# Kernel tuning notes

Measured on AMD Instinct MI355X. Metric: run time of the kernel, lower is better.

The kernel has to match this reference:

```python
import jax, jax.numpy as jnp
import numpy as np

N = 100000
E = 600000
D = 128
D_OUT = 128
NUM_CONV = 3


def setup_inputs() -> dict:
    key = jax.random.key(0)
    k0, k1, k2, k3, k4, k5 = jax.random.split(key, 6)
    x = jax.random.normal(k0, (N, D), dtype=jnp.float32)
    edge_index = jax.random.randint(k1, (2, E), 0, N, dtype=jnp.int64)
    s = 1.0 / np.sqrt(D)
    W = jax.random.uniform(k2, (D, D), minval=-s, maxval=s, dtype=jnp.float32)
    b = jax.random.uniform(k3, (D,), minval=-s, maxval=s, dtype=jnp.float32)
    W_out = jax.random.uniform(k4, (D, D_OUT), minval=-s, maxval=s, dtype=jnp.float32)
    b_out = jax.random.uniform(k5, (D_OUT,), minval=-s, maxval=s, dtype=jnp.float32)
    return {"x": x, "edge_index": edge_index, "W": W, "b": b,
            "W_out": W_out, "b_out": b_out}


def reference(x, edge_index, W, b, W_out, b_out):
    src, dst = edge_index[0], edge_index[1]
    for _ in range(NUM_CONV):
        # gather messages from src nodes, scatter-sum into dst nodes
        agg = jax.ops.segment_sum(x[src], dst, num_segments=N)  # [N, D]
        x = jax.nn.relu(agg @ W + b)  # shared GCNLayer weights + ReLU
    return x @ W_out + b_out  # [N, D_OUT]
```

## Files before the change

### kernel.cpp

```cpp
#include <hip/hip_runtime.h>

#define NN 100000
#define NE 600000
#define DD 128

typedef __attribute__((ext_vector_type(8))) short bf16x8;
typedef __attribute__((ext_vector_type(4))) float f32x4;

__device__ __forceinline__ ushort f2bf(float f) {
  uint u = __float_as_uint(f);
  return (ushort)((u + 0x7FFF + ((u >> 16) & 1)) >> 16);
}
__device__ __forceinline__ float bf2f(ushort h) { return __uint_as_float(((uint)h) << 16); }


__global__ __launch_bounds__(256) void zero_kernel(int* __restrict__ p, int n) {
  int i = blockIdx.x * 256 + threadIdx.x;
  if (i < n) p[i] = 0;
}

__global__ __launch_bounds__(256) void count_deg(const int* __restrict__ dst, int* __restrict__ cnt) {
  int e = blockIdx.x * 256 + threadIdx.x;
  if (e < NE) atomicAdd(&cnt[dst[e]], 1);
}

__global__ __launch_bounds__(1024) void scan_partial(const int* __restrict__ cnt,
                                                     int* __restrict__ rowptr,
                                                     int* __restrict__ bsum) {
  __shared__ int tmp[2][1024];
  int t = threadIdx.x;
  int g = blockIdx.x * 1024 + t;
  int v = (g < NN) ? cnt[g] : 0;
  tmp[0][t] = v;
  __syncthreads();
  int pb = 0;
  for (int off = 1; off < 1024; off <<= 1) {
    int nv = tmp[pb][t] + ((t >= off) ? tmp[pb][t - off] : 0);
    tmp[1 - pb][t] = nv;
    pb ^= 1;
    __syncthreads();
  }
  int incl = tmp[pb][t];
  if (g < NN) rowptr[g] = incl - v;
  if (t == 1023) bsum[blockIdx.x] = incl;
}

__global__ __launch_bounds__(128) void scan_sums(int* __restrict__ bsum, int nb) {
  __shared__ int s[128];
  int t = threadIdx.x;
  s[t] = (t < nb) ? bsum[t] : 0;
  __syncthreads();
  if (t == 0) {
    int run = 0;
    for (int j = 0; j < nb; ++j) { int v = s[j]; s[j] = run; run += v; }
  }
  __syncthreads();
  if (t < nb) bsum[t] = s[t];
}

__global__ __launch_bounds__(256) void scan_add(int* __restrict__ rowptr, const int* __restrict__ bsum) {
  int g = blockIdx.x * 256 + threadIdx.x;
  if (g < NN) rowptr[g] += bsum[g >> 10];
  if (g == 0) rowptr[NN] = NE;
}

__global__ __launch_bounds__(256) void fill_csr(const int* __restrict__ src, const int* __restrict__ dst,
                                                const int* __restrict__ rowptr, int* __restrict__ cur,
                                                int* __restrict__ srcidx) {
  int e = blockIdx.x * 256 + threadIdx.x;
  if (e < NE) {
    int d = dst[e];
    int pos = atomicAdd(&cur[d], 1);
    srcidx[rowptr[d] + pos] = src[e];
  }
}


__global__ __launch_bounds__(256) void wprep(const float* __restrict__ W, const float* __restrict__ Wo,
                                             ushort* __restrict__ WTh, ushort* __restrict__ WTl,
                                             ushort* __restrict__ WToh, ushort* __restrict__ WTol) {
  int i = blockIdx.x * 256 + threadIdx.x;
  int j = i & 16383;
  int k = j >> 7, n = j & 127;
  float w = (i < 16384) ? W[j] : Wo[j];
  ushort h = f2bf(w);
  ushort lo = f2bf(w - bf2f(h));
  int o = n * 128 + k;
  if (i < 16384) { WTh[o] = h; WTl[o] = lo; }
  else           { WToh[o] = h; WTol[o] = lo; }
}


__global__ __launch_bounds__(256) void aggregate(const float* __restrict__ y,
                                                 const int* __restrict__ rowptr,
                                                 const int* __restrict__ srcidx,
                                                 ushort* __restrict__ Ah, ushort* __restrict__ Al) {
  int grp  = (int)((blockIdx.x * 256 + threadIdx.x) >> 5);
  int lane = threadIdx.x & 31;
  if (grp >= NN) return;
  int beg = rowptr[grp], end = rowptr[grp + 1];
  float4 a0 = make_float4(0.f, 0.f, 0.f, 0.f);
  float4 a1 = make_float4(0.f, 0.f, 0.f, 0.f);
  int j = beg;
  for (; j + 2 <= end; j += 2) {
    int s0 = srcidx[j], s1 = srcidx[j + 1];
    float4 v0 = *(const float4*)(y + (size_t)s0 * DD + lane * 4);
    float4 v1 = *(const float4*)(y + (size_t)s1 * DD + lane * 4);
    a0.x += v0.x; a0.y += v0.y; a0.z += v0.z; a0.w += v0.w;
    a1.x += v1.x; a1.y += v1.y; a1.z += v1.z; a1.w += v1.w;
  }
  if (j < end) {
    int s0 = srcidx[j];
    float4 v0 = *(const float4*)(y + (size_t)s0 * DD + lane * 4);
    a0.x += v0.x; a0.y += v0.y; a0.z += v0.z; a0.w += v0.w;
  }
  float v[4] = {a0.x + a1.x, a0.y + a1.y, a0.z + a1.z, a0.w + a1.w};
  ushort h[4], l[4];
  #pragma unroll
  for (int r = 0; r < 4; ++r) { h[r] = f2bf(v[r]); l[r] = f2bf(v[r] - bf2f(h[r])); }
  uint2 hh, ll;
  hh.x = (uint)h[0] | ((uint)h[1] << 16); hh.y = (uint)h[2] | ((uint)h[3] << 16);
  ll.x = (uint)l[0] | ((uint)l[1] << 16); ll.y = (uint)l[2] | ((uint)l[3] << 16);
  *(uint2*)(Ah + (size_t)grp * DD + lane * 4) = hh;
  *(uint2*)(Al + (size_t)grp * DD + lane * 4) = ll;
}


template <int MODE>
__global__ __launch_bounds__(256, 3) void gemm_mfma(const ushort* Ah, const ushort* Al,
                                                    const ushort* __restrict__ Bh, const ushort* __restrict__ Bl,
                                                    const float* __restrict__ bias,
                                                    float* Cf, ushort* Ch, ushort* Cl, int nrows) {
  __shared__ ushort BHs[128 * 64];
  __shared__ ushort BLs[128 * 64];
  int t = threadIdx.x;
  int w = t >> 6, l = t & 63;
  int lrow = l & 15, g = l >> 4;
  int m0 = blockIdx.x * 128 + w * 32;

  f32x4 acc[2][8];
  #pragma unroll
  for (int rt = 0; rt < 2; ++rt)
    #pragma unroll
    for (int ct = 0; ct < 8; ++ct) acc[rt][ct] = (f32x4){0.f, 0.f, 0.f, 0.f};

  #pragma unroll
  for (int p = 0; p < 2; ++p) {
    #pragma unroll
    for (int i = 0; i < 4; ++i) {
      int c = t + i * 256;
      int n = c >> 3, k8 = c & 7;
      int gsrc = n * 128 + p * 64 + k8 * 8;
      int dsw  = n * 64 + (((k8 * 16) ^ ((n & 7) << 4)) >> 1);
      *(uint4*)(&BHs[dsw]) = *(const uint4*)(Bh + gsrc);
      *(uint4*)(&BLs[dsw]) = *(const uint4*)(Bl + gsrc);
    }
    __syncthreads();

    #pragma unroll
    for (int kb = 0; kb < 2; ++kb) {
      int kgl = (p * 2 + kb) * 32 + g * 8;
      bf16x8 ah[2], al[2];
      #pragma unroll
      for (int rt = 0; rt < 2; ++rt) {
        int row = m0 + rt * 16 + lrow; if (row >= nrows) row = nrows - 1;
        ah[rt] = *(const bf16x8*)(Ah + (size_t)row * DD + kgl);
        al[rt] = *(const bf16x8*)(Al + (size_t)row * DD + kgl);
      }
      int kloc = kb * 64 + g * 16;
      int swz = (lrow & 7) << 4;
      #pragma unroll
      for (int ct = 0; ct < 8; ++ct) {
        int off = (ct * 16 + lrow) * 64 + ((kloc ^ swz) >> 1);
        bf16x8 bh = *(const bf16x8*)(&BHs[off]);
        bf16x8 bl = *(const bf16x8*)(&BLs[off]);
        #pragma unroll
        for (int rt = 0; rt < 2; ++rt) {
          acc[rt][ct] = __builtin_amdgcn_mfma_f32_16x16x32_bf16(ah[rt], bh, acc[rt][ct], 0, 0, 0);
          acc[rt][ct] = __builtin_amdgcn_mfma_f32_16x16x32_bf16(ah[rt], bl, acc[rt][ct], 0, 0, 0);
          acc[rt][ct] = __builtin_amdgcn_mfma_f32_16x16x32_bf16(al[rt], bh, acc[rt][ct], 0, 0, 0);
        }
      }
    }
    __syncthreads();
  }

  float bb[8];
  #pragma unroll
  for (int ct = 0; ct < 8; ++ct) bb[ct] = bias[ct * 16 + lrow];
  #pragma unroll
  for (int rt = 0; rt < 2; ++rt) {
    #pragma unroll
    for (int r = 0; r < 4; ++r) {
      int row = m0 + rt * 16 + g * 4 + r;
      if (row < nrows) {
        #pragma unroll
        for (int ct = 0; ct < 8; ++ct) {
          float v = acc[rt][ct][r] + bb[ct];
          if (MODE != 2) v = fmaxf(v, 0.f);
          int col = ct * 16 + lrow;
          if (MODE == 1) {
            ushort h = f2bf(v);
            Ch[(size_t)row * DD + col] = h;
            Cl[(size_t)row * DD + col] = f2bf(v - bf2f(h));
          } else {
            Cf[(size_t)row * DD + col] = v;
          }
        }
      }
    }
  }
}


extern "C" void kernel_launch(void* const* d_in, const int* in_sizes, int n_in,
                              void* d_out, int out_size, void* d_ws, size_t ws_size,
                              hipStream_t stream) {
  const float* x     = (const float*)d_in[0];
  const int*   ei    = (const int*)d_in[1];
  const float* W     = (const float*)d_in[2];
  const float* b     = (const float*)d_in[3];
  const float* W_out = (const float*)d_in[4];
  const float* b_out = (const float*)d_in[5];
  float*       out   = (float*)d_out;

  const int* src = ei;
  const int* dst = ei + NE;

  char* ws = (char*)d_ws;
  int*    rowptr = (int*)(ws + 0);
  int*    cnt    = (int*)(ws + 400128);
  int*    bsum   = (int*)(ws + 800256);
  int*    srcidx = (int*)(ws + 802304);
  ushort* WTh    = (ushort*)(ws + 3202304);
  ushort* WTl    = (ushort*)(ws + 3235072);
  ushort* WToh   = (ushort*)(ws + 3267840);
  ushort* WTol   = (ushort*)(ws + 3300608);
  ushort* Ahb    = (ushort*)(ws + 3333376);
  ushort* Alb    = (ushort*)(ws + 28933376);
  float*  yf     = (float*)(ws + 54533376);

  const int nb_scan = (NN + 1023) / 1024;

  zero_kernel<<<(NN + 255) / 256, 256, 0, stream>>>(cnt, NN);
  count_deg<<<(NE + 255) / 256, 256, 0, stream>>>(dst, cnt);
  scan_partial<<<nb_scan, 1024, 0, stream>>>(cnt, rowptr, bsum);
  scan_sums<<<1, 128, 0, stream>>>(bsum, nb_scan);
  scan_add<<<(NN + 255) / 256, 256, 0, stream>>>(rowptr, bsum);
  zero_kernel<<<(NN + 255) / 256, 256, 0, stream>>>(cnt, NN);
  fill_csr<<<(NE + 255) / 256, 256, 0, stream>>>(src, dst, rowptr, cnt, srcidx);
  wprep<<<128, 256, 0, stream>>>(W, W_out, WTh, WTl, WToh, WTol);

  const int aggBlocks  = (NN * 32 + 255) / 256;
  const int gemmBlocks = (NN + 127) / 128;

  aggregate<<<aggBlocks, 256, 0, stream>>>(x, rowptr, srcidx, Ahb, Alb);
  gemm_mfma<0><<<gemmBlocks, 256, 0, stream>>>(Ahb, Alb, WTh, WTl, b, yf, nullptr, nullptr, NN);
  aggregate<<<aggBlocks, 256, 0, stream>>>(yf, rowptr, srcidx, Ahb, Alb);
  gemm_mfma<0><<<gemmBlocks, 256, 0, stream>>>(Ahb, Alb, WTh, WTl, b, yf, nullptr, nullptr, NN);
  aggregate<<<aggBlocks, 256, 0, stream>>>(yf, rowptr, srcidx, Ahb, Alb);
  gemm_mfma<1><<<gemmBlocks, 256, 0, stream>>>(Ahb, Alb, WTh, WTl, b, nullptr, Ahb, Alb, NN);
  gemm_mfma<2><<<gemmBlocks, 256, 0, stream>>>(Ahb, Alb, WToh, WTol, b_out, out, nullptr, nullptr, NN);
}
```

Measured before the change: 413.6 us.

## Fuse aggregation with GEMM per layer and merge setup kernels

Each GCN layer now runs as one kernel: a 512-thread block gathers and sums neighbour rows for 128 nodes, splits them into bf16 hi/lo parts and stores them in swizzled LDS, then runs the MFMA GEMM straight from LDS with bias and ReLU. The last layer also chains the output projection inside the same kernel. This removes the round-trip of the bf16 hi/lo intermediates through global memory and cuts several launches. Setup is trimmed too: the weight prep is merged into the counter-zeroing kernel, and the CSR fill counts down with atomicSub so the second zeroing pass can go. In exchange, B fragments now come from global/L2 instead of LDS, each block holds 64KB of LDS, which limits occupancy, and the gather phase gives each warp more rows to process serially.

```diff
diff --git a/kernel.cpp b/kernel.cpp
--- a/kernel.cpp
+++ b/kernel.cpp
@@ -14,9 +14,23 @@
 __device__ __forceinline__ float bf2f(ushort h) { return __uint_as_float(((uint)h) << 16); }
 
 
-__global__ __launch_bounds__(256) void zero_kernel(int* __restrict__ p, int n) {
+__global__ __launch_bounds__(256) void zero_wprep(int* __restrict__ cnt,
+                                                  const float* __restrict__ W, const float* __restrict__ Wo,
+                                                  ushort* __restrict__ WTh, ushort* __restrict__ WTl,
+                                                  ushort* __restrict__ WToh, ushort* __restrict__ WTol) {
   int i = blockIdx.x * 256 + threadIdx.x;
-  if (i < n) p[i] = 0;
+  if (i < NN) cnt[i] = 0;
+  int j = i - NN;
+  if (j >= 0 && j < 32768) {
+    int q = j & 16383;
+    int k = q >> 7, n = q & 127;
+    float w = (j < 16384) ? W[q] : Wo[q];
+    ushort h = f2bf(w);
+    ushort lo = f2bf(w - bf2f(h));
+    int o = n * 128 + k;
+    if (j < 16384) { WTh[o] = h; WTl[o] = lo; }
+    else           { WToh[o] = h; WTol[o] = lo; }
+  }
 }
 
 __global__ __launch_bounds__(256) void count_deg(const int* __restrict__ dst, int* __restrict__ cnt) {
@@ -70,143 +84,149 @@
   int e = blockIdx.x * 256 + threadIdx.x;
   if (e < NE) {
     int d = dst[e];
-    int pos = atomicAdd(&cur[d], 1);
+    int pos = atomicSub(&cur[d], 1) - 1;
     srcidx[rowptr[d] + pos] = src[e];
   }
 }
 
 
-__global__ __launch_bounds__(256) void wprep(const float* __restrict__ W, const float* __restrict__ Wo,
-                                             ushort* __restrict__ WTh, ushort* __restrict__ WTl,
-                                             ushort* __restrict__ WToh, ushort* __restrict__ WTol) {
-  int i = blockIdx.x * 256 + threadIdx.x;
-  int j = i & 16383;
-  int k = j >> 7, n = j & 127;
-  float w = (i < 16384) ? W[j] : Wo[j];
-  ushort h = f2bf(w);
-  ushort lo = f2bf(w - bf2f(h));
-  int o = n * 128 + k;
-  if (i < 16384) { WTh[o] = h; WTl[o] = lo; }
-  else           { WToh[o] = h; WTol[o] = lo; }
-}
-
-
-__global__ __launch_bounds__(256) void aggregate(const float* __restrict__ y,
-                                                 const int* __restrict__ rowptr,
-                                                 const int* __restrict__ srcidx,
-                                                 ushort* __restrict__ Ah, ushort* __restrict__ Al) {
-  int grp  = (int)((blockIdx.x * 256 + threadIdx.x) >> 5);
-  int lane = threadIdx.x & 31;
-  if (grp >= NN) return;
-  int beg = rowptr[grp], end = rowptr[grp + 1];
-  float4 a0 = make_float4(0.f, 0.f, 0.f, 0.f);
-  float4 a1 = make_float4(0.f, 0.f, 0.f, 0.f);
-  int j = beg;
-  for (; j + 2 <= end; j += 2) {
-    int s0 = srcidx[j], s1 = srcidx[j + 1];
-    float4 v0 = *(const float4*)(y + (size_t)s0 * DD + lane * 4);
-    float4 v1 = *(const float4*)(y + (size_t)s1 * DD + lane * 4);
-    a0.x += v0.x; a0.y += v0.y; a0.z += v0.z; a0.w += v0.w;
-    a1.x += v1.x; a1.y += v1.y; a1.z += v1.z; a1.w += v1.w;
-  }
-  if (j < end) {
-    int s0 = srcidx[j];
-    float4 v0 = *(const float4*)(y + (size_t)s0 * DD + lane * 4);
-    a0.x += v0.x; a0.y += v0.y; a0.z += v0.z; a0.w += v0.w;
-  }
-  float v[4] = {a0.x + a1.x, a0.y + a1.y, a0.z + a1.z, a0.w + a1.w};
-  ushort h[4], l[4];
-  #pragma unroll
-  for (int r = 0; r < 4; ++r) { h[r] = f2bf(v[r]); l[r] = f2bf(v[r] - bf2f(h[r])); }
-  uint2 hh, ll;
-  hh.x = (uint)h[0] | ((uint)h[1] << 16); hh.y = (uint)h[2] | ((uint)h[3] << 16);
-  ll.x = (uint)l[0] | ((uint)l[1] << 16); ll.y = (uint)l[2] | ((uint)l[3] << 16);
-  *(uint2*)(Ah + (size_t)grp * DD + lane * 4) = hh;
-  *(uint2*)(Al + (size_t)grp * DD + lane * 4) = ll;
-}
-
-
-template <int MODE>
-__global__ __launch_bounds__(256, 3) void gemm_mfma(const ushort* Ah, const ushort* Al,
-                                                    const ushort* __restrict__ Bh, const ushort* __restrict__ Bl,
-                                                    const float* __restrict__ bias,
-                                                    float* Cf, ushort* Ch, ushort* Cl, int nrows) {
-  __shared__ ushort BHs[128 * 64];
-  __shared__ ushort BLs[128 * 64];
-  int t = threadIdx.x;
+template <bool LAST>
+__global__ __launch_bounds__(512, 4) void layer_fused(
+    const float* __restrict__ yin,
+    const int* __restrict__ rowptr, const int* __restrict__ srcidx,
+    const ushort* __restrict__ Bh, const ushort* __restrict__ Bl,
+    const float* __restrict__ bias,
+    const ushort* __restrict__ B2h, const ushort* __restrict__ B2l,
+    const float* __restrict__ bias2,
+    float* __restrict__ yout) {
+  __shared__ ushort AH[128 * 128];
+  __shared__ ushort AL[128 * 128];
+  int t  = threadIdx.x;
+  int m0 = blockIdx.x * 128;
+
+  {
+    int gp = t >> 5, lane = t & 31;
+    for (int rr = 0; rr < 8; ++rr) {
+      int row  = gp * 8 + rr;
+      int node = m0 + row;
+      float4 a0 = make_float4(0.f, 0.f, 0.f, 0.f);
+      float4 a1 = make_float4(0.f, 0.f, 0.f, 0.f);
+      if (node < NN) {
+        int beg = rowptr[node], end = rowptr[node + 1];
+        int j = beg;
+        for (; j + 2 <= end; j += 2) {
+          int s0 = srcidx[j], s1 = srcidx[j + 1];
+          float4 v0 = *(const float4*)(yin + (size_t)s0 * DD + lane * 4);
+          float4 v1 = *(const float4*)(yin + (size_t)s1 * DD + lane * 4);
+          a0.x += v0.x; a0.y += v0.y; a0.z += v0.z; a0.w += v0.w;
+          a1.x += v1.x; a1.y += v1.y; a1.z += v1.z; a1.w += v1.w;
+        }
+        if (j < end) {
+          int s0 = srcidx[j];
+          float4 v0 = *(const float4*)(yin + (size_t)s0 * DD + lane * 4);
+          a0.x += v0.x; a0.y += v0.y; a0.z += v0.z; a0.w += v0.w;
+        }
+      }
+      float v[4] = {a0.x + a1.x, a0.y + a1.y, a0.z + a1.z, a0.w + a1.w};
+      ushort h[4], l[4];
+      #pragma unroll
+      for (int r = 0; r < 4; ++r) { h[r] = f2bf(v[r]); l[r] = f2bf(v[r] - bf2f(h[r])); }
+      uint2 hh, ll;
+      hh.x = (uint)h[0] | ((uint)h[1] << 16); hh.y = (uint)h[2] | ((uint)h[3] << 16);
+      ll.x = (uint)l[0] | ((uint)l[1] << 16); ll.y = (uint)l[2] | ((uint)l[3] << 16);
+      int boff = row * 256 + ((lane * 8) ^ ((row & 7) << 4));
+      *(uint2*)((char*)AH + boff) = hh;
+      *(uint2*)((char*)AL + boff) = ll;
+    }
+  }
+  __syncthreads();
+
   int w = t >> 6, l = t & 63;
   int lrow = l & 15, g = l >> 4;
-  int m0 = blockIdx.x * 128 + w * 32;
-
-  f32x4 acc[2][8];
+  int rbase = w * 16;
+
+  bf16x8 ah[4], al[4];
   #pragma unroll
-  for (int rt = 0; rt < 2; ++rt)
-    #pragma unroll
-    for (int ct = 0; ct < 8; ++ct) acc[rt][ct] = (f32x4){0.f, 0.f, 0.f, 0.f};
-
+  for (int kb = 0; kb < 4; ++kb) {
+    int row  = rbase + lrow;
+    int boff = row * 256 + ((kb * 64 + g * 16) ^ ((row & 7) << 4));
+    ah[kb] = *(const bf16x8*)((char*)AH + boff);
+    al[kb] = *(const bf16x8*)((char*)AL + boff);
+  }
+  f32x4 acc[8];
   #pragma unroll
-  for (int p = 0; p < 2; ++p) {
-    #pragma unroll
-    for (int i = 0; i < 4; ++i) {
-      int c = t + i * 256;
-      int n = c >> 3, k8 = c & 7;
-      int gsrc = n * 128 + p * 64 + k8 * 8;
-      int dsw  = n * 64 + (((k8 * 16) ^ ((n & 7) << 4)) >> 1);
-      *(uint4*)(&BHs[dsw]) = *(const uint4*)(Bh + gsrc);
-      *(uint4*)(&BLs[dsw]) = *(const uint4*)(Bl + gsrc);
-    }
+  for (int ct = 0; ct < 8; ++ct) acc[ct] = (f32x4){0.f, 0.f, 0.f, 0.f};
+
+  #pragma unroll
+  for (int ct = 0; ct < 8; ++ct) {
+    int nrow = ct * 16 + lrow;
+    #pragma unroll
+    for (int kb = 0; kb < 4; ++kb) {
+      bf16x8 bh = *(const bf16x8*)(Bh + (size_t)nrow * 128 + kb * 32 + g * 8);
+      bf16x8 bl = *(const bf16x8*)(Bl + (size_t)nrow * 128 + kb * 32 + g * 8);
+      acc[ct] = __builtin_amdgcn_mfma_f32_16x16x32_bf16(ah[kb], bh, acc[ct], 0, 0, 0);
+      acc[ct] = __builtin_amdgcn_mfma_f32_16x16x32_bf16(ah[kb], bl, acc[ct], 0, 0, 0);
+      acc[ct] = __builtin_amdgcn_mfma_f32_16x16x32_bf16(al[kb], bh, acc[ct], 0, 0, 0);
+    }
+  }
+
+  if (!LAST) {
+    #pragma unroll
+    for (int ct = 0; ct < 8; ++ct) {
+      float bb = bias[ct * 16 + lrow];
+      #pragma unroll
+      for (int r = 0; r < 4; ++r) {
+        int row = m0 + rbase + g * 4 + r;
+        if (row < NN) {
+          float v = fmaxf(acc[ct][r] + bb, 0.f);
+          yout[(size_t)row * DD + ct * 16 + lrow] = v;
+        }
+      }
+    }
+  } else {
     __syncthreads();
-
-    #pragma unroll
-    for (int kb = 0; kb < 2; ++kb) {
-      int kgl = (p * 2 + kb) * 32 + g * 8;
-      bf16x8 ah[2], al[2];
-      #pragma unroll
-      for (int rt = 0; rt < 2; ++rt) {
-        int row = m0 + rt * 16 + lrow; if (row >= nrows) row = nrows - 1;
-        ah[rt] = *(const bf16x8*)(Ah + (size_t)row * DD + kgl);
-        al[rt] = *(const bf16x8*)(Al + (size_t)row * DD + kgl);
-      }
-      int kloc = kb * 64 + g * 16;
-      int swz = (lrow & 7) << 4;
-      #pragma unroll
-      for (int ct = 0; ct < 8; ++ct) {
-        int off = (ct * 16 + lrow) * 64 + ((kloc ^ swz) >> 1);
-        bf16x8 bh = *(const bf16x8*)(&BHs[off]);
-        bf16x8 bl = *(const bf16x8*)(&BLs[off]);
-        #pragma unroll
-        for (int rt = 0; rt < 2; ++rt) {
-          acc[rt][ct] = __builtin_amdgcn_mfma_f32_16x16x32_bf16(ah[rt], bh, acc[rt][ct], 0, 0, 0);
-          acc[rt][ct] = __builtin_amdgcn_mfma_f32_16x16x32_bf16(ah[rt], bl, acc[rt][ct], 0, 0, 0);
-          acc[rt][ct] = __builtin_amdgcn_mfma_f32_16x16x32_bf16(al[rt], bh, acc[rt][ct], 0, 0, 0);
-        }
+    #pragma unroll
+    for (int ct = 0; ct < 8; ++ct) {
+      float bb = bias[ct * 16 + lrow];
+      #pragma unroll
+      for (int r = 0; r < 4; ++r) {
+        float v = fmaxf(acc[ct][r] + bb, 0.f);
+        ushort h  = f2bf(v);
+        ushort lo = f2bf(v - bf2f(h));
+        int row  = rbase + g * 4 + r;
+        int boff = row * 256 + (((ct * 16 + lrow) * 2) ^ ((row & 7) << 4));
+        *(ushort*)((char*)AH + boff) = h;
+        *(ushort*)((char*)AL + boff) = lo;
       }
     }
     __syncthreads();
-  }
-
-  float bb[8];
-  #pragma unroll
-  for (int ct = 0; ct < 8; ++ct) bb[ct] = bias[ct * 16 + lrow];
-  #pragma unroll
-  for (int rt = 0; rt < 2; ++rt) {
-    #pragma unroll
-    for (int r = 0; r < 4; ++r) {
-      int row = m0 + rt * 16 + g * 4 + r;
-      if (row < nrows) {
-        #pragma unroll
-        for (int ct = 0; ct < 8; ++ct) {
-          float v = acc[rt][ct][r] + bb[ct];
-          if (MODE != 2) v = fmaxf(v, 0.f);
-          int col = ct * 16 + lrow;
-          if (MODE == 1) {
-            ushort h = f2bf(v);
-            Ch[(size_t)row * DD + col] = h;
-            Cl[(size_t)row * DD + col] = f2bf(v - bf2f(h));
-          } else {
-            Cf[(size_t)row * DD + col] = v;
-          }
-        }
+
+    f32x4 acc2[8];
+    #pragma unroll
+    for (int ct = 0; ct < 8; ++ct) acc2[ct] = (f32x4){0.f, 0.f, 0.f, 0.f};
+    #pragma unroll
+    for (int ct = 0; ct < 8; ++ct) {
+      int nrow = ct * 16 + lrow;
+      #pragma unroll
+      for (int kb = 0; kb < 4; ++kb) {
+        int row  = rbase + lrow;
+        int boff = row * 256 + ((kb * 64 + g * 16) ^ ((row & 7) << 4));
+        bf16x8 ch = *(const bf16x8*)((char*)AH + boff);
+        bf16x8 cl = *(const bf16x8*)((char*)AL + boff);
+        bf16x8 bh = *(const bf16x8*)(B2h + (size_t)nrow * 128 + kb * 32 + g * 8);
+        bf16x8 bl = *(const bf16x8*)(B2l + (size_t)nrow * 128 + kb * 32 + g * 8);
+        acc2[ct] = __builtin_amdgcn_mfma_f32_16x16x32_bf16(ch, bh, acc2[ct], 0, 0, 0);
+        acc2[ct] = __builtin_amdgcn_mfma_f32_16x16x32_bf16(ch, bl, acc2[ct], 0, 0, 0);
+        acc2[ct] = __builtin_amdgcn_mfma_f32_16x16x32_bf16(cl, bh, acc2[ct], 0, 0, 0);
+      }
+    }
+    #pragma unroll
+    for (int ct = 0; ct < 8; ++ct) {
+      float bb = bias2[ct * 16 + lrow];
+      #pragma unroll
+      for (int r = 0; r < 4; ++r) {
+        int row = m0 + rbase + g * 4 + r;
+        if (row < NN) yout[(size_t)row * DD + ct * 16 + lrow] = acc2[ct][r] + bb;
       }
     }
   }
@@ -236,29 +256,24 @@
   ushort* WTl    = (ushort*)(ws + 3235072);
   ushort* WToh   = (ushort*)(ws + 3267840);
   ushort* WTol   = (ushort*)(ws + 3300608);
-  ushort* Ahb    = (ushort*)(ws + 3333376);
-  ushort* Alb    = (ushort*)(ws + 28933376);
-  float*  yf     = (float*)(ws + 54533376);
+  float*  yf1    = (float*)(ws + 3333376);
+  float*  yf2    = (float*)(ws + 54533376);
 
   const int nb_scan = (NN + 1023) / 1024;
 
-  zero_kernel<<<(NN + 255) / 256, 256, 0, stream>>>(cnt, NN);
+  zero_wprep<<<(NN + 32768 + 255) / 256, 256, 0, stream>>>(cnt, W, W_out, WTh, WTl, WToh, WTol);
   count_deg<<<(NE + 255) / 256, 256, 0, stream>>>(dst, cnt);
   scan_partial<<<nb_scan, 1024, 0, stream>>>(cnt, rowptr, bsum);
   scan_sums<<<1, 128, 0, stream>>>(bsum, nb_scan);
   scan_add<<<(NN + 255) / 256, 256, 0, stream>>>(rowptr, bsum);
-  zero_kernel<<<(NN + 255) / 256, 256, 0, stream>>>(cnt, NN);
   fill_csr<<<(NE + 255) / 256, 256, 0, stream>>>(src, dst, rowptr, cnt, srcidx);
-  wprep<<<128, 256, 0, stream>>>(W, W_out, WTh, WTl, WToh, WTol);
-
-  const int aggBlocks  = (NN * 32 + 255) / 256;
-  const int gemmBlocks = (NN + 127) / 128;
-
-  aggregate<<<aggBlocks, 256, 0, stream>>>(x, rowptr, srcidx, Ahb, Alb);
-  gemm_mfma<0><<<gemmBlocks, 256, 0, stream>>>(Ahb, Alb, WTh, WTl, b, yf, nullptr, nullptr, NN);
-  aggregate<<<aggBlocks, 256, 0, stream>>>(yf, rowptr, srcidx, Ahb, Alb);
-  gemm_mfma<0><<<gemmBlocks, 256, 0, stream>>>(Ahb, Alb, WTh, WTl, b, yf, nullptr, nullptr, NN);
-  aggregate<<<aggBlocks, 256, 0, stream>>>(yf, rowptr, srcidx, Ahb, Alb);
-  gemm_mfma<1><<<gemmBlocks, 256, 0, stream>>>(Ahb, Alb, WTh, WTl, b, nullptr, Ahb, Alb, NN);
-  gemm_mfma<2><<<gemmBlocks, 256, 0, stream>>>(Ahb, Alb, WToh, WTol, b_out, out, nullptr, nullptr, NN);
-}
+
+  const int lblocks = (NN + 127) / 128;
+
+  layer_fused<false><<<lblocks, 512, 0, stream>>>(x,   rowptr, srcidx, WTh, WTl, b,
+                                                  nullptr, nullptr, nullptr, yf1);
+  layer_fused<false><<<lblocks, 512, 0, stream>>>(yf1, rowptr, srcidx, WTh, WTl, b,
+                                                  nullptr, nullptr, nullptr, yf2);
+  layer_fused<true><<<lblocks, 512, 0, stream>>>(yf2, rowptr, srcidx, WTh, WTl, b,
+                                                 WToh, WTol, b_out, out);
+}
```

After: 591.7 us. +43.1%, slower.
